# Optimization experiments

Hardware: AMD Instinct MI355X
Metric: run time of the kernel (lower is better)

## Reference

```python
import jax, jax.numpy as jnp
import numpy as np

B, C, H, W = 4, 256, 64, 64

def _conv1x1(x, Wt, b):
    # x: [b,c,h,w], Wt: [out,in], b: [out]
    return jnp.einsum('bchw,dc->bdhw', x, Wt) + b[None, :, None, None]

def setup_inputs() -> dict:
    key = jax.random.key(0)
    ks = jax.random.split(key, 10)
    s = 1.0 / np.sqrt(C)
    return {
        'F_c': jax.random.normal(ks[0], (B, C, H, W), jnp.float32),
        'F_s': jax.random.normal(ks[1], (B, C, H, W), jnp.float32),
        'Wf': jax.random.normal(ks[2], (C, C), jnp.float32) * s,
        'bf': jnp.zeros((C,), jnp.float32),
        'Wg': jax.random.normal(ks[3], (C, C), jnp.float32) * s,
        'bg': jnp.zeros((C,), jnp.float32),
        'Wh': jax.random.normal(ks[4], (C, C), jnp.float32) * s,
        'bh': jnp.zeros((C,), jnp.float32),
        'Wo': jax.random.normal(ks[5], (C, C), jnp.float32) * s,
        'bo': jnp.zeros((C,), jnp.float32),
    }

def reference(F_c, F_s, Wf, bf, Wg, bg, Wh, bh, Wo, bo):
    b, c, h, w = F_c.shape
    Fq = _conv1x1(F_c, Wf, bf).reshape(b, c, -1)          # [b,c,Nc]
    G = _conv1x1(F_s, Wg, bg).reshape(b, c, -1)           # [b,c,Ns]
    Hv = _conv1x1(F_s, Wh, bh).reshape(b, c, -1)          # [b,c,Ns]
    S = jnp.einsum('bcn,bcm->bnm', Fq, G)                 # [b,Nc,Ns] (unscaled)
    S = jax.nn.softmax(S, axis=-1)
    res = jnp.einsum('bcm,bnm->bcn', Hv, S)               # [b,c,Nc]
    res = res.reshape(b, c, h, w)
    return _conv1x1(res, Wo, bo)
```

## Files before the change

kernel.cpp:

```cpp
#include <hip/hip_runtime.h>
#include <stdint.h>

#define NB 4
#define CC 256
#define NN 4096
#define KITERS 32
#define WAIT_LGKM0 0xC07F

typedef __attribute__((ext_vector_type(8))) _Float16 half8;
typedef __attribute__((ext_vector_type(4))) _Float16 half4;
typedef __attribute__((ext_vector_type(2))) _Float16 half2v;
typedef __attribute__((ext_vector_type(4))) float floatx4;
typedef __attribute__((ext_vector_type(16))) float float16v;
typedef __attribute__((ext_vector_type(4))) int intx4;

__device__ __forceinline__ void cvt16v(float4 a, float4 b, float4 c, float4 d,
                                       half8& lo, half8& hi) {
  lo[0] = (_Float16)a.x; lo[1] = (_Float16)a.y; lo[2] = (_Float16)a.z; lo[3] = (_Float16)a.w;
  lo[4] = (_Float16)b.x; lo[5] = (_Float16)b.y; lo[6] = (_Float16)b.z; lo[7] = (_Float16)b.w;
  hi[0] = (_Float16)c.x; hi[1] = (_Float16)c.y; hi[2] = (_Float16)c.z; hi[3] = (_Float16)c.w;
  hi[4] = (_Float16)d.x; hi[5] = (_Float16)d.y; hi[6] = (_Float16)d.z; hi[7] = (_Float16)d.w;
}

__global__ __launch_bounds__(256, 3) void k_qkv(const float* __restrict__ Fc,
                                                const float* __restrict__ Fs,
                                                const float* __restrict__ Wf,
                                                const float* __restrict__ Wg,
                                                const float* __restrict__ Wh,
                                                const float* __restrict__ bf,
                                                const float* __restrict__ bg,
                                                const float* __restrict__ bh,
                                                _Float16* __restrict__ Qs,
                                                _Float16* __restrict__ Ks,
                                                _Float16* __restrict__ Vs) {
  __shared__ float tmp[32][132];
  __shared__ _Float16 As[128][40];
  __shared__ _Float16 Bs[128][40];
  const int z = blockIdx.z, bz = blockIdx.y;
  const float* F = ((z == 0) ? Fc : Fs) + (size_t)bz * CC * NN;
  const float* W = (z == 0) ? Wf : ((z == 1) ? Wg : Wh);
  const float* bias = (z == 0) ? bf : ((z == 1) ? bg : bh);
  int mt, nt;
  if (z < 2) { mt = blockIdx.x >> 5; nt = blockIdx.x & 31; }
  else       { mt = blockIdx.x >> 1; nt = blockIdx.x & 1;  }
  const int m0 = mt * 128, n0 = nt * 128;
  const int xn0 = (z < 2) ? n0 : m0;
  const int wd0 = (z < 2) ? m0 : n0;
  const int tid = threadIdx.x;
  const int wave = tid >> 6, lane = tid & 63, quad = lane >> 4, l15 = lane & 15;
  const int wm = (wave >> 1) * 64, wn = (wave & 1) * 64;

  floatx4 acc[4][4];
#pragma unroll
  for (int i = 0; i < 4; i++)
#pragma unroll
    for (int j = 0; j < 4; j++) acc[i][j] = (floatx4){0.f, 0.f, 0.f, 0.f};

  const int srow = tid >> 1, shalf = (tid & 1) * 16;
  const int fc = tid >> 3, fn = (tid & 7) * 16;
  const int xr = tid >> 1, xh = (tid & 1) * 16;

  float4 wr0, wr1, wr2, wr3, fr0, fr1, fr2, fr3;
  {
    const float4* wp = (const float4*)(W + (size_t)(wd0 + srow) * 256 + 0 + shalf);
    wr0 = wp[0]; wr1 = wp[1]; wr2 = wp[2]; wr3 = wp[3];
    const float4* fp = (const float4*)(F + (size_t)(0 + fc) * NN + xn0 + fn);
    fr0 = fp[0]; fr1 = fp[1]; fr2 = fp[2]; fr3 = fp[3];
  }

  for (int kk = 0; kk < 256; kk += 32) {
    __syncthreads();
    *(float4*)&tmp[fc][fn + 0] = fr0;
    *(float4*)&tmp[fc][fn + 4] = fr1;
    *(float4*)&tmp[fc][fn + 8] = fr2;
    *(float4*)&tmp[fc][fn + 12] = fr3;
    half8 w_lo, w_hi;
    cvt16v(wr0, wr1, wr2, wr3, w_lo, w_hi);
    if (z < 2) {
      *(half8*)&As[srow][shalf] = w_lo;
      *(half8*)&As[srow][shalf + 8] = w_hi;
    } else {
      *(half8*)&Bs[srow][shalf] = w_lo;
      *(half8*)&Bs[srow][shalf + 8] = w_hi;
    }
    __syncthreads();
    if (kk + 32 < 256) {
      const float4* wp = (const float4*)(W + (size_t)(wd0 + srow) * 256 + kk + 32 + shalf);
      wr0 = wp[0]; wr1 = wp[1]; wr2 = wp[2]; wr3 = wp[3];
      const float4* fp = (const float4*)(F + (size_t)(kk + 32 + fc) * NN + xn0 + fn);
      fr0 = fp[0]; fr1 = fp[1]; fr2 = fp[2]; fr3 = fp[3];
    }
    half8 xlo, xhi;
#pragma unroll
    for (int i = 0; i < 8; i++) xlo[i] = (_Float16)tmp[xh + i][xr];
#pragma unroll
    for (int i = 0; i < 8; i++) xhi[i] = (_Float16)tmp[xh + 8 + i][xr];
    if (z < 2) {
      *(half8*)&Bs[xr][xh] = xlo;
      *(half8*)&Bs[xr][xh + 8] = xhi;
    } else {
      *(half8*)&As[xr][xh] = xlo;
      *(half8*)&As[xr][xh + 8] = xhi;
    }
    __syncthreads();
    half8 af[4], bfr[4];
#pragma unroll
    for (int mb = 0; mb < 4; mb++) af[mb] = *(const half8*)&As[wm + mb * 16 + l15][quad * 8];
#pragma unroll
    for (int nb = 0; nb < 4; nb++) bfr[nb] = *(const half8*)&Bs[wn + nb * 16 + l15][quad * 8];
#pragma unroll
    for (int mb = 0; mb < 4; mb++)
#pragma unroll
      for (int nb = 0; nb < 4; nb++)
        acc[mb][nb] = __builtin_amdgcn_mfma_f32_16x16x32_f16(af[mb], bfr[nb], acc[mb][nb], 0, 0, 0);
  }

  if (z < 2) {
    _Float16* op = (z == 0 ? Qs : Ks) + (size_t)bz * NN * CC;
#pragma unroll
    for (int mb = 0; mb < 4; mb++) {
      int d0 = m0 + wm + mb * 16 + quad * 4;
      float b0 = bias[d0], b1 = bias[d0 + 1], b2 = bias[d0 + 2], b3 = bias[d0 + 3];
      const int cs = d0 >> 4, hh = (d0 >> 3) & 1, j0 = d0 & 7;
#pragma unroll
      for (int nb = 0; nb < 4; nb++) {
        int n_ = n0 + wn + nb * 16 + l15;
        int kt = n_ >> 5, ql_ = n_ & 31;
        half4 pk;
        pk[0] = (_Float16)(acc[mb][nb][0] + b0);
        pk[1] = (_Float16)(acc[mb][nb][1] + b1);
        pk[2] = (_Float16)(acc[mb][nb][2] + b2);
        pk[3] = (_Float16)(acc[mb][nb][3] + b3);
        size_t idx = ((size_t)(kt * 16 + cs) * 64 + ql_ + 32 * hh) * 8 + j0;
        *(half4*)(op + idx) = pk;
      }
    }
  } else {
    _Float16* op = Vs + (size_t)bz * NN * CC;
#pragma unroll
    for (int mb = 0; mb < 4; mb++) {
      int nq0 = m0 + wm + mb * 16 + quad * 4;
      const int kt = nq0 >> 5, krel = nq0 & 31;
      const int hk = krel >> 4, hh = (krel >> 3) & 1, j0 = krel & 7;
#pragma unroll
      for (int nb = 0; nb < 4; nb++) {
        int d = n0 + wn + nb * 16 + l15;
        int ql_ = d & 31, g = (d >> 5) & 7;
        float bv = bias[d];
        half4 pk;
        pk[0] = (_Float16)(acc[mb][nb][0] + bv);
        pk[1] = (_Float16)(acc[mb][nb][1] + bv);
        pk[2] = (_Float16)(acc[mb][nb][2] + bv);
        pk[3] = (_Float16)(acc[mb][nb][3] + bv);
        size_t idx = (((size_t)(kt * 8 + g) * 2 + hk) * 64 + ql_ + 32 * hh) * 8 + j0;
        *(half4*)(op + idx) = pk;
      }
    }
  }
}

__global__ __launch_bounds__(256, 2) void k_attn(const _Float16* __restrict__ Q,
                                                 const _Float16* __restrict__ K,
                                                 const _Float16* __restrict__ Vt,
                                                 _Float16* __restrict__ Opart,
                                                 float2* __restrict__ Ml) {
  __shared__ _Float16 smem[8192 * 3 + 4096];
  const int tid = threadIdx.x;
  const int wave = tid >> 6, lane = tid & 63;
  _Float16* Kl = smem;
  _Float16* Plw = smem + 3 * 8192 + wave * 1024;

  const int qt = blockIdx.x, ck = blockIdx.y, b = blockIdx.z;
  const int ql = lane & 31, h = lane >> 5;
  const int q0 = qt * 128 + wave * 32;
  const _Float16* Qb = Q + (size_t)b * NN * CC;
  const _Float16* Kb = K + (size_t)b * NN * CC;
  const _Float16* Vb = Vt + (size_t)b * NN * CC;
  const int kt_base = ck * (1024 / 32);

  const int ktq = q0 >> 5;
  half8 qf[16];
#pragma unroll
  for (int cs = 0; cs < 16; cs++)
    qf[cs] = *(const half8*)(Qb + ((size_t)(ktq * 16 + cs) * 64 + lane) * 8);

  float16v Oa[8];
#pragma unroll
  for (int g = 0; g < 8; g++)
#pragma unroll
    for (int i = 0; i < 16; i++) Oa[g][i] = 0.f;

  float m_run = -1e30f, l_run = 0.f;

  intx4 kpre[4], vpre[4];
  {
    const _Float16* Kt = Kb + (size_t)kt_base * 8192;
    const _Float16* Vtile = Vb + (size_t)kt_base * 8192;
#pragma unroll
    for (int p = 0; p < 4; p++) {
      kpre[p] = *(const intx4*)(Kt + tid * 8 + p * 2048);
      vpre[p] = *(const intx4*)(Vtile + tid * 8 + p * 2048);
    }
  }

  for (int t = 0; t < KITERS; t++) {
    const int vb = t & 1;
    _Float16* Vw = smem + (1 + vb) * 8192;
    __syncthreads();
#pragma unroll
    for (int p = 0; p < 4; p++) {
      *(intx4*)(Kl + tid * 8 + p * 2048) = kpre[p];
      *(intx4*)(Vw + tid * 8 + p * 2048) = vpre[p];
    }
    __syncthreads();
    if (t + 1 < KITERS) {
      const _Float16* Kt = Kb + (size_t)(kt_base + t + 1) * 8192;
      const _Float16* Vtile = Vb + (size_t)(kt_base + t + 1) * 8192;
#pragma unroll
      for (int p = 0; p < 4; p++) {
        kpre[p] = *(const intx4*)(Kt + tid * 8 + p * 2048);
        vpre[p] = *(const intx4*)(Vtile + tid * 8 + p * 2048);
      }
    }

    float16v s, s2;
#pragma unroll
    for (int i = 0; i < 16; i++) { s[i] = 0.f; s2[i] = 0.f; }
    if (t > 0) {
      _Float16* Vr = smem + (1 + (vb ^ 1)) * 8192;
      half8 pf0 = *(const half8*)(Plw + lane * 8);
      half8 pf1 = *(const half8*)(Plw + 512 + lane * 8);
#pragma unroll
      for (int u = 0; u < 8; u++) {
        half8 kfa = *(const half8*)(Kl + (2 * u) * 512 + lane * 8);
        s = __builtin_amdgcn_mfma_f32_32x32x16_f16(kfa, qf[2 * u], s, 0, 0, 0);
        half8 vfa = *(const half8*)(Vr + (u * 2) * 512 + lane * 8);
        Oa[u] = __builtin_amdgcn_mfma_f32_32x32x16_f16(vfa, pf0, Oa[u], 0, 0, 0);
        half8 kfb = *(const half8*)(Kl + (2 * u + 1) * 512 + lane * 8);
        s2 = __builtin_amdgcn_mfma_f32_32x32x16_f16(kfb, qf[2 * u + 1], s2, 0, 0, 0);
        half8 vfb = *(const half8*)(Vr + (u * 2 + 1) * 512 + lane * 8);
        Oa[u] = __builtin_amdgcn_mfma_f32_32x32x16_f16(vfb, pf1, Oa[u], 0, 0, 0);
      }
    } else {
#pragma unroll
      for (int cs = 0; cs < 16; cs += 2) {
        half8 kfa = *(const half8*)(Kl + cs * 512 + lane * 8);
        s = __builtin_amdgcn_mfma_f32_32x32x16_f16(kfa, qf[cs], s, 0, 0, 0);
        half8 kfb = *(const half8*)(Kl + (cs + 1) * 512 + lane * 8);
        s2 = __builtin_amdgcn_mfma_f32_32x32x16_f16(kfb, qf[cs + 1], s2, 0, 0, 0);
      }
    }
#pragma unroll
    for (int i = 0; i < 16; i++) s[i] += s2[i];

    float t0 = fmaxf(s[0], s[1]), t1 = fmaxf(s[2], s[3]);
    float t2 = fmaxf(s[4], s[5]), t3 = fmaxf(s[6], s[7]);
    float t4 = fmaxf(s[8], s[9]), t5 = fmaxf(s[10], s[11]);
    float t6 = fmaxf(s[12], s[13]), t7 = fmaxf(s[14], s[15]);
    t0 = fmaxf(t0, t1); t2 = fmaxf(t2, t3); t4 = fmaxf(t4, t5); t6 = fmaxf(t6, t7);
    float tmax = fmaxf(fmaxf(t0, t2), fmaxf(t4, t6));
    tmax = fmaxf(tmax, __shfl_xor(tmax, 32));
    bool need = tmax > m_run + 8.0f;
    if (__any((int)need)) {
      float mN = need ? tmax : m_run;
      float alpha = __expf(m_run - mN);
      m_run = mN;
      l_run *= alpha;
#pragma unroll
      for (int g = 0; g < 8; g++)
#pragma unroll
        for (int i = 0; i < 16; i++) Oa[g][i] *= alpha;
    }
#pragma unroll
    for (int i = 0; i < 16; i++) s[i] = __expf(s[i] - m_run);
    float u0 = (s[0] + s[1]) + (s[2] + s[3]);
    float u1 = (s[4] + s[5]) + (s[6] + s[7]);
    float u2 = (s[8] + s[9]) + (s[10] + s[11]);
    float u3 = (s[12] + s[13]) + (s[14] + s[15]);
    float ts = (u0 + u1) + (u2 + u3);
    ts += __shfl_xor(ts, 32);
    l_run += ts;
#pragma unroll
    for (int r = 0; r < 16; r += 2) {
      half2v pk;
      pk[0] = (_Float16)s[r];
      pk[1] = (_Float16)s[r + 1];
      int k = (r & 3) + 8 * (r >> 2) + 4 * h;
      *(half2v*)(Plw + (k >> 4) * 512 + (ql + 32 * ((k >> 3) & 1)) * 8 + (k & 7)) = pk;
    }
  }

  {
    _Float16* Vr = smem + (1 + ((KITERS - 1) & 1)) * 8192;
    half8 pf0 = *(const half8*)(Plw + lane * 8);
    half8 pf1 = *(const half8*)(Plw + 512 + lane * 8);
#pragma unroll
    for (int u = 0; u < 8; u++) {
      half8 vfa = *(const half8*)(Vr + (u * 2) * 512 + lane * 8);
      Oa[u] = __builtin_amdgcn_mfma_f32_32x32x16_f16(vfa, pf0, Oa[u], 0, 0, 0);
      half8 vfb = *(const half8*)(Vr + (u * 2 + 1) * 512 + lane * 8);
      Oa[u] = __builtin_amdgcn_mfma_f32_32x32x16_f16(vfb, pf1, Oa[u], 0, 0, 0);
    }
  }

  float invl = 1.f / l_run;
  __syncthreads();
  float* ot = (float*)smem + wave * (32 * 33);
  _Float16* Opb = Opart + ((size_t)ck * NB + b) * NN * CC;
  const int qr = lane >> 1;
  const int chalf = (lane & 1) * 16;
#pragma unroll
  for (int g = 0; g < 8; g++) {
#pragma unroll
    for (int r = 0; r < 16; r++)
      ot[((r & 3) + 8 * (r >> 2) + 4 * h) * 33 + ql] = Oa[g][r] * invl;
    __builtin_amdgcn_s_waitcnt(WAIT_LGKM0);
    half8 o0, o1;
#pragma unroll
    for (int i = 0; i < 8; i++) o0[i] = (_Float16)ot[(chalf + i) * 33 + qr];
#pragma unroll
    for (int i = 0; i < 8; i++) o1[i] = (_Float16)ot[(chalf + 8 + i) * 33 + qr];
    _Float16* gp = Opb + (size_t)(q0 + qr) * CC + g * 32 + chalf;
    *(half8*)gp = o0;
    *(half8*)(gp + 8) = o1;
    __builtin_amdgcn_s_waitcnt(WAIT_LGKM0);
  }
  if (h == 0) {
    float2 ml; ml.x = m_run; ml.y = l_run;
    Ml[((size_t)ck * NB + b) * NN + q0 + ql] = ml;
  }
}

__global__ __launch_bounds__(256, 2) void k_out(const _Float16* __restrict__ Opart,
                                                const float2* __restrict__ Ml,
                                                const float* __restrict__ Wo,
                                                const float* __restrict__ bo,
                                                float* __restrict__ out) {
  __shared__ _Float16 As[128][40];
  __shared__ _Float16 Bs[128][40];
  const int bz = blockIdx.y;
  const int mt = blockIdx.x >> 1, nt = blockIdx.x & 1;
  const int m0 = mt * 128, n0 = nt * 128;
  const int tid = threadIdx.x;
  const int wave = tid >> 6, lane = tid & 63, quad = lane >> 4, l15 = lane & 15;
  const int wm = (wave >> 1) * 64, wn = (wave & 1) * 64;

  floatx4 acc[4][4];
#pragma unroll
  for (int i = 0; i < 4; i++)
#pragma unroll
    for (int j = 0; j < 4; j++) acc[i][j] = (floatx4){0.f, 0.f, 0.f, 0.f};

  const int srow = tid >> 1;
  const int shalf = (tid & 1) * 16;

  const size_t qi = (size_t)bz * NN + m0 + srow;
  float2 a0 = Ml[qi], a1 = Ml[(size_t)NB * NN + qi];
  float2 a2 = Ml[(size_t)2 * NB * NN + qi], a3 = Ml[(size_t)3 * NB * NN + qi];
  float M = fmaxf(fmaxf(a0.x, a1.x), fmaxf(a2.x, a3.x));
  float w0 = __expf(a0.x - M) * a0.y, w1 = __expf(a1.x - M) * a1.y;
  float w2 = __expf(a2.x - M) * a2.y, w3 = __expf(a3.x - M) * a3.y;
  float inv = 1.f / (w0 + w1 + w2 + w3);
  w0 *= inv; w1 *= inv; w2 *= inv; w3 *= inv;
  const size_t ps = (size_t)NB * NN * CC;
  const _Float16* prow = Opart + qi * CC;

  for (int kk = 0; kk < 256; kk += 32) {
    const _Float16* pr = prow + kk + shalf;
    half8 p0a = *(const half8*)pr,            p0b = *(const half8*)(pr + 8);
    half8 p1a = *(const half8*)(pr + ps),     p1b = *(const half8*)(pr + ps + 8);
    half8 p2a = *(const half8*)(pr + 2 * ps), p2b = *(const half8*)(pr + 2 * ps + 8);
    half8 p3a = *(const half8*)(pr + 3 * ps), p3b = *(const half8*)(pr + 3 * ps + 8);
    half8 ma, mb2;
#pragma unroll
    for (int i = 0; i < 8; i++) {
      ma[i] = (_Float16)(w0 * (float)p0a[i] + w1 * (float)p1a[i] +
                         w2 * (float)p2a[i] + w3 * (float)p3a[i]);
      mb2[i] = (_Float16)(w0 * (float)p0b[i] + w1 * (float)p1b[i] +
                          w2 * (float)p2b[i] + w3 * (float)p3b[i]);
    }
    const float4* wp = (const float4*)(Wo + (size_t)(n0 + srow) * 256 + kk + shalf);
    half8 b_lo, b_hi;
    cvt16v(wp[0], wp[1], wp[2], wp[3], b_lo, b_hi);
    __syncthreads();
    *(half8*)&As[srow][shalf] = ma;
    *(half8*)&As[srow][shalf + 8] = mb2;
    *(half8*)&Bs[srow][shalf] = b_lo;
    *(half8*)&Bs[srow][shalf + 8] = b_hi;
    __syncthreads();
    half8 af[4], bfr[4];
#pragma unroll
    for (int mb = 0; mb < 4; mb++) af[mb] = *(const half8*)&As[wm + mb * 16 + l15][quad * 8];
#pragma unroll
    for (int nb = 0; nb < 4; nb++) bfr[nb] = *(const half8*)&Bs[wn + nb * 16 + l15][quad * 8];
#pragma unroll
    for (int mb = 0; mb < 4; mb++)
#pragma unroll
      for (int nb = 0; nb < 4; nb++)
        acc[mb][nb] = __builtin_amdgcn_mfma_f32_16x16x32_f16(af[mb], bfr[nb], acc[mb][nb], 0, 0, 0);
  }

  float* op = out + (size_t)bz * NN * CC;
#pragma unroll
  for (int mb = 0; mb < 4; mb++) {
    int nq0 = m0 + wm + mb * 16 + quad * 4;
#pragma unroll
    for (int nb = 0; nb < 4; nb++) {
      int d = n0 + wn + nb * 16 + l15;
      float bv = bo[d];
      floatx4 pk;
      pk[0] = acc[mb][nb][0] + bv;
      pk[1] = acc[mb][nb][1] + bv;
      pk[2] = acc[mb][nb][2] + bv;
      pk[3] = acc[mb][nb][3] + bv;
      *(floatx4*)(op + (size_t)d * NN + nq0) = pk;
    }
  }
}

extern "C" void kernel_launch(void* const* d_in, const int* in_sizes, int n_in,
                              void* d_out, int out_size, void* d_ws, size_t ws_size,
                              hipStream_t stream) {
  const float* Fc = (const float*)d_in[0];
  const float* Fs = (const float*)d_in[1];
  const float* Wf = (const float*)d_in[2];
  const float* bf_ = (const float*)d_in[3];
  const float* Wg = (const float*)d_in[4];
  const float* bg = (const float*)d_in[5];
  const float* Wh = (const float*)d_in[6];
  const float* bh = (const float*)d_in[7];
  const float* Wo = (const float*)d_in[8];
  const float* bo = (const float*)d_in[9];

  char* ws = (char*)d_ws;
  const size_t sz = (size_t)NB * NN * CC * sizeof(_Float16);
  _Float16* Opart = (_Float16*)(ws + 0 * sz);
  _Float16* Qs = (_Float16*)(ws + 4 * sz);
  _Float16* Ks = (_Float16*)(ws + 5 * sz);
  _Float16* Vs = (_Float16*)(ws + 6 * sz);
  float2* Ml = (float2*)(ws + 7 * sz);

  k_qkv<<<dim3(64, NB, 3), 256, 0, stream>>>(Fc, Fs, Wf, Wg, Wh, bf_, bg, bh, Qs, Ks, Vs);
  k_attn<<<dim3(32, 4, NB), 256, 0, stream>>>(Qs, Ks, Vs, Opart, Ml);
  k_out<<<dim3(64, NB), 256, 0, stream>>>(Opart, Ml, Wo, bo, (float*)d_out);
}
```

Before: 212.1 us.

## Shrink k_out M-tile, prefetch next K-slice into registers, reorder attn MFMA interleave

The output-projection kernel now uses a 64-row M tile instead of 128. That doubles the grid to 128x4 blocks for better CU occupancy, and each wave computes a 64x32 sub-tile. Loads of the next K-slice of the partial outputs and Wo are issued into registers before the MFMAs of the current slice, to hide global latency behind compute. The attention inner loop is reordered so each K-fragment MFMA is followed by a V MFMA in a flat 16-step loop, and the tail PV loop is split into two passes. The smaller tile re-reads Wo more often and keeps more prefetched values live in registers.

Result: no change. 211.7 us (-0.2%).

```diff
diff --git a/kernel.cpp b/kernel.cpp
--- a/kernel.cpp
+++ b/kernel.cpp
@@ -231,15 +231,15 @@
       half8 pf0 = *(const half8*)(Plw + lane * 8);
       half8 pf1 = *(const half8*)(Plw + 512 + lane * 8);
 #pragma unroll
-      for (int u = 0; u < 8; u++) {
-        half8 kfa = *(const half8*)(Kl + (2 * u) * 512 + lane * 8);
-        s = __builtin_amdgcn_mfma_f32_32x32x16_f16(kfa, qf[2 * u], s, 0, 0, 0);
-        half8 vfa = *(const half8*)(Vr + (u * 2) * 512 + lane * 8);
-        Oa[u] = __builtin_amdgcn_mfma_f32_32x32x16_f16(vfa, pf0, Oa[u], 0, 0, 0);
-        half8 kfb = *(const half8*)(Kl + (2 * u + 1) * 512 + lane * 8);
-        s2 = __builtin_amdgcn_mfma_f32_32x32x16_f16(kfb, qf[2 * u + 1], s2, 0, 0, 0);
-        half8 vfb = *(const half8*)(Vr + (u * 2 + 1) * 512 + lane * 8);
-        Oa[u] = __builtin_amdgcn_mfma_f32_32x32x16_f16(vfb, pf1, Oa[u], 0, 0, 0);
+      for (int i = 0; i < 16; i++) {
+        half8 kf = *(const half8*)(Kl + i * 512 + lane * 8);
+        if (i & 1)
+          s2 = __builtin_amdgcn_mfma_f32_32x32x16_f16(kf, qf[i], s2, 0, 0, 0);
+        else
+          s = __builtin_amdgcn_mfma_f32_32x32x16_f16(kf, qf[i], s, 0, 0, 0);
+        const int u = i & 7, ks = i >> 3;
+        half8 vf = *(const half8*)(Vr + (2 * u + ks) * 512 + lane * 8);
+        Oa[u] = __builtin_amdgcn_mfma_f32_32x32x16_f16(vf, ks ? pf1 : pf0, Oa[u], 0, 0, 0);
       }
     } else {
 #pragma unroll
@@ -296,9 +296,12 @@
     half8 pf1 = *(const half8*)(Plw + 512 + lane * 8);
 #pragma unroll
     for (int u = 0; u < 8; u++) {
-      half8 vfa = *(const half8*)(Vr + (u * 2) * 512 + lane * 8);
+      half8 vfa = *(const half8*)(Vr + (2 * u) * 512 + lane * 8);
       Oa[u] = __builtin_amdgcn_mfma_f32_32x32x16_f16(vfa, pf0, Oa[u], 0, 0, 0);
-      half8 vfb = *(const half8*)(Vr + (u * 2 + 1) * 512 + lane * 8);
+    }
+#pragma unroll
+    for (int u = 0; u < 8; u++) {
+      half8 vfb = *(const half8*)(Vr + (2 * u + 1) * 512 + lane * 8);
       Oa[u] = __builtin_amdgcn_mfma_f32_32x32x16_f16(vfb, pf1, Oa[u], 0, 0, 0);
     }
   }
@@ -336,25 +339,25 @@
                                                 const float* __restrict__ Wo,
                                                 const float* __restrict__ bo,
                                                 float* __restrict__ out) {
-  __shared__ _Float16 As[128][40];
+  __shared__ _Float16 As[64][40];
   __shared__ _Float16 Bs[128][40];
   const int bz = blockIdx.y;
   const int mt = blockIdx.x >> 1, nt = blockIdx.x & 1;
-  const int m0 = mt * 128, n0 = nt * 128;
+  const int m0 = mt * 64, n0 = nt * 128;
   const int tid = threadIdx.x;
   const int wave = tid >> 6, lane = tid & 63, quad = lane >> 4, l15 = lane & 15;
-  const int wm = (wave >> 1) * 64, wn = (wave & 1) * 64;
-
-  floatx4 acc[4][4];
+  const int wn = wave * 32;
+
+  floatx4 acc[4][2];
 #pragma unroll
   for (int i = 0; i < 4; i++)
 #pragma unroll
-    for (int j = 0; j < 4; j++) acc[i][j] = (floatx4){0.f, 0.f, 0.f, 0.f};
-
-  const int srow = tid >> 1;
-  const int shalf = (tid & 1) * 16;
-
-  const size_t qi = (size_t)bz * NN + m0 + srow;
+    for (int j = 0; j < 2; j++) acc[i][j] = (floatx4){0.f, 0.f, 0.f, 0.f};
+
+  const int arow = tid >> 2, acol = (tid & 3) * 8;
+  const int brow = tid >> 1, bcol = (tid & 1) * 16;
+
+  const size_t qi = (size_t)bz * NN + m0 + arow;
   float2 a0 = Ml[qi], a1 = Ml[(size_t)NB * NN + qi];
   float2 a2 = Ml[(size_t)2 * NB * NN + qi], a3 = Ml[(size_t)3 * NB * NN + qi];
   float M = fmaxf(fmaxf(a0.x, a1.x), fmaxf(a2.x, a3.x));
@@ -365,47 +368,58 @@
   const size_t ps = (size_t)NB * NN * CC;
   const _Float16* prow = Opart + qi * CC;
 
+  half8 pA0, pA1, pA2, pA3;
+  float4 wr0, wr1, wr2, wr3;
+  {
+    const _Float16* pr = prow + acol;
+    pA0 = *(const half8*)pr;
+    pA1 = *(const half8*)(pr + ps);
+    pA2 = *(const half8*)(pr + 2 * ps);
+    pA3 = *(const half8*)(pr + 3 * ps);
+    const float4* wp = (const float4*)(Wo + (size_t)(n0 + brow) * 256 + bcol);
+    wr0 = wp[0]; wr1 = wp[1]; wr2 = wp[2]; wr3 = wp[3];
+  }
+
   for (int kk = 0; kk < 256; kk += 32) {
-    const _Float16* pr = prow + kk + shalf;
-    half8 p0a = *(const half8*)pr,            p0b = *(const half8*)(pr + 8);
-    half8 p1a = *(const half8*)(pr + ps),     p1b = *(const half8*)(pr + ps + 8);
-    half8 p2a = *(const half8*)(pr + 2 * ps), p2b = *(const half8*)(pr + 2 * ps + 8);
-    half8 p3a = *(const half8*)(pr + 3 * ps), p3b = *(const half8*)(pr + 3 * ps + 8);
-    half8 ma, mb2;
-#pragma unroll
-    for (int i = 0; i < 8; i++) {
-      ma[i] = (_Float16)(w0 * (float)p0a[i] + w1 * (float)p1a[i] +
-                         w2 * (float)p2a[i] + w3 * (float)p3a[i]);
-      mb2[i] = (_Float16)(w0 * (float)p0b[i] + w1 * (float)p1b[i] +
-                          w2 * (float)p2b[i] + w3 * (float)p3b[i]);
-    }
-    const float4* wp = (const float4*)(Wo + (size_t)(n0 + srow) * 256 + kk + shalf);
+    half8 ma;
+#pragma unroll
+    for (int i = 0; i < 8; i++)
+      ma[i] = (_Float16)(w0 * (float)pA0[i] + w1 * (float)pA1[i] +
+                         w2 * (float)pA2[i] + w3 * (float)pA3[i]);
     half8 b_lo, b_hi;
-    cvt16v(wp[0], wp[1], wp[2], wp[3], b_lo, b_hi);
-    __syncthreads();
-    *(half8*)&As[srow][shalf] = ma;
-    *(half8*)&As[srow][shalf + 8] = mb2;
-    *(half8*)&Bs[srow][shalf] = b_lo;
-    *(half8*)&Bs[srow][shalf + 8] = b_hi;
-    __syncthreads();
-    half8 af[4], bfr[4];
-#pragma unroll
-    for (int mb = 0; mb < 4; mb++) af[mb] = *(const half8*)&As[wm + mb * 16 + l15][quad * 8];
-#pragma unroll
-    for (int nb = 0; nb < 4; nb++) bfr[nb] = *(const half8*)&Bs[wn + nb * 16 + l15][quad * 8];
+    cvt16v(wr0, wr1, wr2, wr3, b_lo, b_hi);
+    __syncthreads();
+    *(half8*)&As[arow][acol] = ma;
+    *(half8*)&Bs[brow][bcol] = b_lo;
+    *(half8*)&Bs[brow][bcol + 8] = b_hi;
+    __syncthreads();
+    if (kk + 32 < 256) {
+      const _Float16* pr = prow + kk + 32 + acol;
+      pA0 = *(const half8*)pr;
+      pA1 = *(const half8*)(pr + ps);
+      pA2 = *(const half8*)(pr + 2 * ps);
+      pA3 = *(const half8*)(pr + 3 * ps);
+      const float4* wp = (const float4*)(Wo + (size_t)(n0 + brow) * 256 + kk + 32 + bcol);
+      wr0 = wp[0]; wr1 = wp[1]; wr2 = wp[2]; wr3 = wp[3];
+    }
+    half8 af[4], bfr[2];
+#pragma unroll
+    for (int mb = 0; mb < 4; mb++) af[mb] = *(const half8*)&As[mb * 16 + l15][quad * 8];
+#pragma unroll
+    for (int nb = 0; nb < 2; nb++) bfr[nb] = *(const half8*)&Bs[wn + nb * 16 + l15][quad * 8];
 #pragma unroll
     for (int mb = 0; mb < 4; mb++)
 #pragma unroll
-      for (int nb = 0; nb < 4; nb++)
+      for (int nb = 0; nb < 2; nb++)
         acc[mb][nb] = __builtin_amdgcn_mfma_f32_16x16x32_f16(af[mb], bfr[nb], acc[mb][nb], 0, 0, 0);
   }
 
   float* op = out + (size_t)bz * NN * CC;
 #pragma unroll
   for (int mb = 0; mb < 4; mb++) {
-    int nq0 = m0 + wm + mb * 16 + quad * 4;
-#pragma unroll
-    for (int nb = 0; nb < 4; nb++) {
+    int nq0 = m0 + mb * 16 + quad * 4;
+#pragma unroll
+    for (int nb = 0; nb < 2; nb++) {
       int d = n0 + wn + nb * 16 + l15;
       float bv = bo[d];
       floatx4 pk;
@@ -442,5 +456,5 @@
 
   k_qkv<<<dim3(64, NB, 3), 256, 0, stream>>>(Fc, Fs, Wf, Wg, Wh, bf_, bg, bh, Qs, Ks, Vs);
   k_attn<<<dim3(32, 4, NB), 256, 0, stream>>>(Qs, Ks, Vs, Opart, Ml);
-  k_out<<<dim3(64, NB), 256, 0, stream>>>(Opart, Ml, Wo, bo, (float*)d_out);
+  k_out<<<dim3(128, NB), 256, 0, stream>>>(Opart, Ml, Wo, bo, (float*)d_out);
 }
```
